# Kernel tuning notes

Hardware: AMD Instinct MI355X
Metric: run time of the kernel (lower is better)

The kernel has to match this reference:

```python
import jax, jax.numpy as jnp
import numpy as np

# Config constants (match init_kwargs)
H = 1024   # hidden_size
F = 4096   # intermediate_size
E = 8      # num_moe_experts
K = 2      # moe_router_topk
S, B = 1024, 2  # seq_len, micro-batch


def setup_inputs() -> dict:
    key = jax.random.key(0)
    ks = jax.random.split(key, 6)
    return {
        "hidden_states": jax.random.normal(ks[0], (S, B, H), jnp.float32),
        "router_w": jax.random.normal(ks[1], (H, E), jnp.float32) * 0.02,
        "w1": jax.random.normal(ks[2], (E, H, F), jnp.float32) * 0.02,
        "b1": jax.random.normal(ks[3], (E, F), jnp.float32) * 0.02,
        "w2": jax.random.normal(ks[4], (E, F, H), jnp.float32) * 0.02,
        "b2": jax.random.normal(ks[5], (E, H), jnp.float32) * 0.02,
    }


def reference(hidden_states, router_w, w1, b1, w2, b2):
    S_, B_, H_ = hidden_states.shape
    x = hidden_states.reshape(-1, H_)                      # [N, H]
    N = x.shape[0]

    # --- TopKRouter (aux_loss routing): topk over logits, softmax over top-k logits ---
    logits = x @ router_w                                  # [N, E]
    top_logits, indices = jax.lax.top_k(logits, K)         # [N, K]
    scores = jax.nn.softmax(top_logits.astype(jnp.float32), axis=-1).astype(logits.dtype)

    # Combine weights [N, E]: scatter top-k scores into expert slots.
    combine = jnp.zeros((N, E), x.dtype).at[jnp.arange(N)[:, None], indices].add(scores)

    # --- Experts: per-expert GPTNeoXMLP (dense over all tokens; math-equivalent
    # to dispatch (token_permutation) + grouped GEMM + scatter_add combine
    # (token_unpermutation) with score weighting for topk>1) ---
    h = jax.nn.gelu(jnp.einsum('nh,ehf->enf', x, w1) + b1[:, None, :], approximate=False)
    y = jnp.einsum('enf,efh->enh', h, w2) + b2[:, None, :]  # [E, N, H]

    out = jnp.einsum('ne,enh->nh', combine, y)              # weighted combine
    return out.reshape(S_, B_, H_)
```

## Files before the change

### kernel.cpp

```cpp
#include <hip/hip_runtime.h>
#include <cmath>


#define H_DIM 1024
#define F_DIM 4096
#define E_NUM 8
#define N_TOK 2048
#define BK 64
#define MAX_SLOTS 5120
#define MAX_MT (MAX_SLOTS / 128)

typedef short s16x8 __attribute__((ext_vector_type(8)));
typedef float f32x4 __attribute__((ext_vector_type(4)));

__device__ __forceinline__ unsigned short f2bf(float f) {
  unsigned int u = __float_as_uint(f);
  u += 0x7fffu + ((u >> 16) & 1u);
  return (unsigned short)(u >> 16);
}

__device__ __forceinline__ void gload_lds16(const void* g, void* l) {
  __builtin_amdgcn_global_load_lds(
      (const __attribute__((address_space(1))) unsigned int*)g,
      (__attribute__((address_space(3))) unsigned int*)l, 16, 0, 0);
}

__device__ __forceinline__ int xcd_swz(int orig, int nwg) {
  const int cpx = nwg >> 3;
  return (orig & 7) * cpx + (orig >> 3);
}

__device__ __forceinline__ float fast_gelu(float v) {
  const float w = v * (1.0f + 0.044715f * v * v);
  const float t = __expf(-1.5957691216f * w);
  return v / (1.0f + t);
}

__device__ __forceinline__ void tcvt_tile(const float* __restrict__ in,
                                          unsigned short* __restrict__ out,
                                          int R, int C, int tile, float (*T)[65]) {
  const int ctiles = C >> 6;
  const int per_e = ctiles * (R >> 6);
  const int e = tile / per_e;
  const int rem = tile - e * per_e;
  const int r0 = (rem / ctiles) << 6;
  const int c0 = (rem % ctiles) << 6;
  const size_t eb = (size_t)e * R * C;
  in += eb; out += eb;
  const int t = threadIdx.x;
  const int cb = (t & 15) * 4;
#pragma unroll
  for (int it = 0; it < 4; ++it) {
    const int rr = (t >> 4) + it * 16;
    f32x4 v = *(const f32x4*)(in + (size_t)(r0 + rr) * C + c0 + cb);
#pragma unroll
    for (int c = 0; c < 4; ++c) T[rr][cb + c] = v[c];
  }
  __syncthreads();
  const int cc = t >> 2;
  const int rb = (t & 3) * 16;
#pragma unroll
  for (int half = 0; half < 2; ++half) {
    s16x8 u;
#pragma unroll
    for (int j = 0; j < 8; ++j) u[j] = (short)f2bf(T[rb + half * 8 + j][cc]);
    *(s16x8*)&out[(size_t)(c0 + cc) * R + r0 + rb + half * 8] = u;
  }
}

__global__ __launch_bounds__(256) void prep1_k(
    const float* __restrict__ w1, unsigned short* __restrict__ wt1,
    const float* __restrict__ x, unsigned short* __restrict__ xb,
    const float* __restrict__ rw, int* __restrict__ meta,
    int* __restrict__ topk_e, float* __restrict__ topk_s) {
  __shared__ float T[64][65];
  const int b = blockIdx.x;
  const int t = threadIdx.x;
  if (b < 8192) {
    tcvt_tile(w1, wt1, H_DIM, F_DIM, b, T);
    return;
  }
  if (b < 9216) {
    const size_t i = (((size_t)(b - 8192)) * 256 + t) * 8;
    f32x4 a = *(const f32x4*)(x + i);
    f32x4 c = *(const f32x4*)(x + i + 4);
    s16x8 u;
#pragma unroll
    for (int j = 0; j < 4; ++j) { u[j] = (short)f2bf(a[j]); u[4 + j] = (short)f2bf(c[j]); }
    *(s16x8*)&xb[i] = u;
    return;
  }
  const int n = (b - 9216) * 4 + (t >> 6);
  const int l = t & 63;
  float part[E_NUM];
#pragma unroll
  for (int e = 0; e < E_NUM; ++e) part[e] = 0.f;
  const float* xr = x + (size_t)n * H_DIM;
  for (int h = l; h < H_DIM; h += 64) {
    const float xv = xr[h];
    const float* rwr = rw + h * E_NUM;
#pragma unroll
    for (int e = 0; e < E_NUM; ++e) part[e] += xv * rwr[e];
  }
#pragma unroll
  for (int e = 0; e < E_NUM; ++e) {
#pragma unroll
    for (int off = 32; off > 0; off >>= 1) part[e] += __shfl_down(part[e], off);
  }
  if (l == 0) {
    float v0 = -3.4e38f, v1 = -3.4e38f;
    int i0 = 0, i1 = 0;
#pragma unroll
    for (int e = 0; e < E_NUM; ++e) {
      float v = part[e];
      if (v > v0) { v1 = v0; i1 = i0; v0 = v; i0 = e; }
      else if (v > v1) { v1 = v; i1 = e; }
    }
    const float e1 = expf(v1 - v0);
    const float inv = 1.f / (1.f + e1);
    topk_e[2 * n] = i0; topk_e[2 * n + 1] = i1;
    topk_s[2 * n] = inv; topk_s[2 * n + 1] = e1 * inv;
    atomicAdd(&meta[i0], 1);
    atomicAdd(&meta[i1], 1);
  }
}

__global__ __launch_bounds__(256) void scatter_k(
    int* __restrict__ meta, const int* __restrict__ topk_e,
    const float* __restrict__ topk_s, int* __restrict__ slot_token,
    float* __restrict__ slot_score) {
  __shared__ int soff[9];
  __shared__ int scur[8];
  const int t = threadIdx.x;
  if (t == 0) {
    int acc = 0;
    for (int e = 0; e < E_NUM; ++e) {
      soff[e] = acc;
      meta[8 + e] = acc;
      acc += ((meta[e] + 127) / 128) * 128;
    }
    soff[8] = acc;
    meta[16] = acc;
  }
  if (t < 8) scur[t] = 0;
  __syncthreads();
  for (int i = t; i < MAX_SLOTS; i += 256) slot_token[i] = -1;
  __syncthreads();
  for (int a = t; a < N_TOK * 2; a += 256) {
    const int e = topk_e[a];
    const int pos = atomicAdd(&scur[e], 1);
    const int slot = soff[e] + pos;
    slot_token[slot] = a >> 1;
    slot_score[slot] = topk_s[a];
  }
}

__global__ __launch_bounds__(256, 2) void gemm1_f(
    const unsigned short* __restrict__ xb, const unsigned short* __restrict__ w1t,
    const float* __restrict__ b1, const int* __restrict__ meta,
    const int* __restrict__ slot_token, unsigned short* __restrict__ hbuf,
    const float* __restrict__ w2, unsigned short* __restrict__ wt2) {
  __shared__ __align__(16) char lraw[65536];
  if (blockIdx.x >= MAX_MT * 32) {
    tcvt_tile(w2, wt2, F_DIM, H_DIM, blockIdx.x - MAX_MT * 32, (float(*)[65])lraw);
    return;
  }
  unsigned short* Al = (unsigned short*)lraw;
  unsigned short* Bl = (unsigned short*)(lraw + 32768);
  const int total = meta[16];
  const int wgid = xcd_swz(blockIdx.x, MAX_MT * 32);
  const int mt = wgid >> 5, nt = wgid & 31;
  const int m0 = mt * 128;
  if (m0 >= total) return;
  int exp = 0;
#pragma unroll
  for (int e = 1; e < E_NUM; ++e) if (m0 >= meta[8 + e]) exp = e;
  const int n0 = nt * 128;
  const int t = threadIdx.x, w = t >> 6, l = t & 63;
  const int wm = w >> 1, wn = w & 1, lr = l & 15, lg = l >> 4;
  const int sr = l >> 3, sc = l & 7;

  const unsigned short* srcA[4];
  const unsigned short* srcB[4];
#pragma unroll
  for (int i = 0; i < 4; ++i) {
    const int r = (w * 4 + i) * 8 + sr;
    const int cd = sc ^ sr;
    int tk = slot_token[m0 + r]; if (tk < 0) tk = 0;
    srcA[i] = xb + (size_t)tk * H_DIM + cd * 8;
    srcB[i] = w1t + ((size_t)exp * F_DIM + n0 + r) * H_DIM + cd * 8;
  }

  const f32x4 fzero = {0.f, 0.f, 0.f, 0.f};
  f32x4 acc[4][4];
#pragma unroll
  for (int a = 0; a < 4; ++a)
#pragma unroll
    for (int b = 0; b < 4; ++b) acc[a][b] = fzero;

#pragma unroll
  for (int i = 0; i < 4; ++i) {
    gload_lds16(srcA[i], Al + (w * 4 + i) * 512);
    gload_lds16(srcB[i], Bl + (w * 4 + i) * 512);
  }
  __syncthreads();
  int cur = 0;
  for (int kt = 0; kt < H_DIM / BK; ++kt) {
    const int nxt = cur ^ 1;
    if (kt + 1 < H_DIM / BK) {
      const int k0 = (kt + 1) * BK;
#pragma unroll
      for (int i = 0; i < 4; ++i) {
        gload_lds16(srcA[i] + k0, Al + nxt * 8192 + (w * 4 + i) * 512);
        gload_lds16(srcB[i] + k0, Bl + nxt * 8192 + (w * 4 + i) * 512);
      }
    }
    const unsigned short* Ac = Al + cur * 8192;
    const unsigned short* Bc = Bl + cur * 8192;
#pragma unroll
    for (int kk = 0; kk < 2; ++kk) {
      s16x8 af[4], bb[4];
#pragma unroll
      for (int fm = 0; fm < 4; ++fm) {
        const int row = wm * 64 + fm * 16 + lr;
        af[fm] = *(const s16x8*)&Ac[row * 64 + (((kk * 4 + lg) ^ (lr & 7)) * 8)];
      }
#pragma unroll
      for (int fn = 0; fn < 4; ++fn) {
        const int row = wn * 64 + fn * 16 + lr;
        bb[fn] = *(const s16x8*)&Bc[row * 64 + (((kk * 4 + lg) ^ (lr & 7)) * 8)];
      }
#pragma unroll
      for (int fm = 0; fm < 4; ++fm)
#pragma unroll
        for (int fn = 0; fn < 4; ++fn)
          acc[fm][fn] = __builtin_amdgcn_mfma_f32_16x16x32_bf16(af[fm], bb[fn], acc[fm][fn], 0, 0, 0);
    }
    __syncthreads();
    cur = nxt;
  }
#pragma unroll
  for (int fn = 0; fn < 4; ++fn) {
    const int col = n0 + wn * 64 + fn * 16 + lr;
    const float bias = b1[exp * F_DIM + col];
#pragma unroll
    for (int fm = 0; fm < 4; ++fm) {
      const int rbase = m0 + wm * 64 + fm * 16 + lg * 4;
#pragma unroll
      for (int i = 0; i < 4; ++i) {
        hbuf[(size_t)(rbase + i) * F_DIM + col] = f2bf(fast_gelu(acc[fm][fn][i] + bias));
      }
    }
  }
}

__global__ __launch_bounds__(256, 2) void gemm2_f(
    const unsigned short* __restrict__ hbuf, const unsigned short* __restrict__ w2t,
    const float* __restrict__ b2, const int* __restrict__ meta,
    const int* __restrict__ slot_token, const float* __restrict__ slot_score,
    float* __restrict__ out) {
  __shared__ __align__(16) char lraw[49152];
  unsigned short* Al = (unsigned short*)lraw;
  unsigned short* Bl = (unsigned short*)(lraw + 32768);
  const int total = meta[16];
  const int wgid = xcd_swz(blockIdx.x, MAX_MT * 16);
  const int mt = wgid >> 4, nt = wgid & 15;
  const int m0 = mt * 128;
  if (m0 >= total) return;
  int exp = 0;
#pragma unroll
  for (int e = 1; e < E_NUM; ++e) if (m0 >= meta[8 + e]) exp = e;
  const int n0 = nt * 64;
  const int t = threadIdx.x, w = t >> 6, l = t & 63;
  const int wm = w >> 1, wn = w & 1, lr = l & 15, lg = l >> 4;
  const int sr = l >> 3, sc = l & 7;

  const unsigned short* srcA[4];
  const unsigned short* srcB[2];
#pragma unroll
  for (int i = 0; i < 4; ++i) {
    const int r = (w * 4 + i) * 8 + sr;
    srcA[i] = hbuf + (size_t)(m0 + r) * F_DIM + (sc ^ sr) * 8;
  }
#pragma unroll
  for (int i = 0; i < 2; ++i) {
    const int r = (w * 2 + i) * 8 + sr;
    srcB[i] = w2t + ((size_t)exp * H_DIM + n0 + r) * F_DIM + (sc ^ sr) * 8;
  }

  const f32x4 fzero = {0.f, 0.f, 0.f, 0.f};
  f32x4 acc[4][2];
#pragma unroll
  for (int a = 0; a < 4; ++a)
#pragma unroll
    for (int b = 0; b < 2; ++b) acc[a][b] = fzero;

#pragma unroll
  for (int i = 0; i < 4; ++i) gload_lds16(srcA[i], Al + (w * 4 + i) * 512);
#pragma unroll
  for (int i = 0; i < 2; ++i) gload_lds16(srcB[i], Bl + (w * 2 + i) * 512);
  __syncthreads();
  int cur = 0;
  for (int kt = 0; kt < F_DIM / BK; ++kt) {
    const int nxt = cur ^ 1;
    if (kt + 1 < F_DIM / BK) {
      const int k0 = (kt + 1) * BK;
#pragma unroll
      for (int i = 0; i < 4; ++i)
        gload_lds16(srcA[i] + k0, Al + nxt * 8192 + (w * 4 + i) * 512);
#pragma unroll
      for (int i = 0; i < 2; ++i)
        gload_lds16(srcB[i] + k0, Bl + nxt * 4096 + (w * 2 + i) * 512);
    }
    const unsigned short* Ac = Al + cur * 8192;
    const unsigned short* Bc = Bl + cur * 4096;
#pragma unroll
    for (int kk = 0; kk < 2; ++kk) {
      s16x8 af[4], bb[2];
#pragma unroll
      for (int fm = 0; fm < 4; ++fm) {
        const int row = wm * 64 + fm * 16 + lr;
        af[fm] = *(const s16x8*)&Ac[row * 64 + (((kk * 4 + lg) ^ (lr & 7)) * 8)];
      }
#pragma unroll
      for (int fn = 0; fn < 2; ++fn) {
        const int row = wn * 32 + fn * 16 + lr;
        bb[fn] = *(const s16x8*)&Bc[row * 64 + (((kk * 4 + lg) ^ (lr & 7)) * 8)];
      }
#pragma unroll
      for (int fm = 0; fm < 4; ++fm)
#pragma unroll
        for (int fn = 0; fn < 2; ++fn)
          acc[fm][fn] = __builtin_amdgcn_mfma_f32_16x16x32_bf16(af[fm], bb[fn], acc[fm][fn], 0, 0, 0);
    }
    __syncthreads();
    cur = nxt;
  }
#pragma unroll
  for (int fm = 0; fm < 4; ++fm) {
    const int rbase = m0 + wm * 64 + fm * 16 + lg * 4;
    int toks[4]; float ss[4];
#pragma unroll
    for (int i = 0; i < 4; ++i) {
      toks[i] = slot_token[rbase + i];
      ss[i] = slot_score[rbase + i];
    }
#pragma unroll
    for (int fn = 0; fn < 2; ++fn) {
      const int col = n0 + wn * 32 + fn * 16 + lr;
      const float b2v = b2[exp * H_DIM + col];
#pragma unroll
      for (int i = 0; i < 4; ++i) {
        if (toks[i] >= 0)
          atomicAdd(out + (size_t)toks[i] * H_DIM + col, ss[i] * (acc[fm][fn][i] + b2v));
      }
    }
  }
}

__global__ __launch_bounds__(256) void tcvt2_k(const float* __restrict__ in,
                                               unsigned short* __restrict__ out) {
  __shared__ float T[64][65];
  tcvt_tile(in, out, F_DIM, H_DIM, blockIdx.x, T);
}

extern "C" void kernel_launch(void* const* d_in, const int* in_sizes, int n_in,
                              void* d_out, int out_size, void* d_ws, size_t ws_size,
                              hipStream_t stream) {
  const float* x  = (const float*)d_in[0];
  const float* rw = (const float*)d_in[1];
  const float* w1 = (const float*)d_in[2];
  const float* b1 = (const float*)d_in[3];
  const float* w2 = (const float*)d_in[4];
  const float* b2 = (const float*)d_in[5];
  float* out = (float*)d_out;
  char* ws = (char*)d_ws;

  int*   meta       = (int*)ws;
  int*   topk_e     = (int*)(ws + 4096);
  float* topk_s     = (float*)(ws + 20480);
  int*   slot_token = (int*)(ws + 36864);
  float* slot_score = (float*)(ws + 57344);
  unsigned short* xb   = (unsigned short*)(ws + (1ull << 20));
  unsigned short* hbuf = (unsigned short*)(ws + (6ull << 20));
  unsigned short* wt1  = (unsigned short*)(ws + (48ull << 20));
  const size_t W = (size_t)E_NUM * H_DIM * F_DIM * 2;
  unsigned short* wt2  = (unsigned short*)(ws + (48ull << 20) + W);
  const size_t NEED_FULL = (48ull << 20) + 2 * W;
  const bool full = ws_size >= NEED_FULL;

  hipMemsetAsync(meta, 0, 256, stream);
  hipMemsetAsync(out, 0, (size_t)N_TOK * H_DIM * sizeof(float), stream);

  prep1_k<<<8192 + 1024 + 512, 256, 0, stream>>>(w1, wt1, x, xb, rw, meta, topk_e, topk_s);
  scatter_k<<<1, 256, 0, stream>>>(meta, topk_e, topk_s, slot_token, slot_score);

  if (full) {
    gemm1_f<<<MAX_MT * 32 + 8192, 256, 0, stream>>>(xb, wt1, b1, meta, slot_token, hbuf, w2, wt2);
    gemm2_f<<<MAX_MT * 16, 256, 0, stream>>>(hbuf, wt2, b2, meta, slot_token, slot_score, out);
  } else {
    gemm1_f<<<MAX_MT * 32, 256, 0, stream>>>(xb, wt1, b1, meta, slot_token, hbuf, w2, wt1);
    tcvt2_k<<<8192, 256, 0, stream>>>(w2, wt1);
    gemm2_f<<<MAX_MT * 16, 256, 0, stream>>>(hbuf, wt1, b2, meta, slot_token, slot_score, out);
  }
}
```

Before: 281.5 us.

## Replace LDS transpose-convert with register-based tiles, memset slot table, raise gemm2 occupancy

The weight transpose-and-bf16-convert no longer stages a 64x64 tile through shared memory. Each thread now reads a column strip of 32 rows into registers and writes 32 contiguous bf16 values, with half as many blocks. This drops LDS use and a barrier from the conversion blocks co-scheduled with gemm1. The slot_token initialization moves from the single-block scatter kernel to a hipMemsetAsync, and gemm2's launch bound asks for 3 blocks per CU. The column-strided global reads may coalesce less well, though each wavefront still reads contiguous rows of 256 floats.

```diff
diff --git a/kernel.cpp b/kernel.cpp
--- a/kernel.cpp
+++ b/kernel.cpp
@@ -9,6 +9,9 @@
 #define BK 64
 #define MAX_SLOTS 5120
 #define MAX_MT (MAX_SLOTS / 128)
+#define G1_GRID (MAX_MT * 32)
+#define G2_GRID (MAX_MT * 16)
+#define TCVT_BLKS 4096
 
 typedef short s16x8 __attribute__((ext_vector_type(8)));
 typedef float f32x4 __attribute__((ext_vector_type(4)));
@@ -36,35 +39,28 @@
   return v / (1.0f + t);
 }
 
-__device__ __forceinline__ void tcvt_tile(const float* __restrict__ in,
+__device__ __forceinline__ void fast_tcvt(const float* __restrict__ in,
                                           unsigned short* __restrict__ out,
-                                          int R, int C, int tile, float (*T)[65]) {
-  const int ctiles = C >> 6;
-  const int per_e = ctiles * (R >> 6);
-  const int e = tile / per_e;
-  const int rem = tile - e * per_e;
-  const int r0 = (rem / ctiles) << 6;
-  const int c0 = (rem % ctiles) << 6;
+                                          int R, int C, int tile) {
+  const int ct = C >> 8;
+  const int nb = (R >> 5) * ct;
+  const int e = tile / nb;
+  const int rem = tile - e * nb;
+  const int r0 = (rem / ct) << 5;
+  const int c0 = (rem % ct) << 8;
   const size_t eb = (size_t)e * R * C;
-  in += eb; out += eb;
-  const int t = threadIdx.x;
-  const int cb = (t & 15) * 4;
-#pragma unroll
-  for (int it = 0; it < 4; ++it) {
-    const int rr = (t >> 4) + it * 16;
-    f32x4 v = *(const f32x4*)(in + (size_t)(r0 + rr) * C + c0 + cb);
-#pragma unroll
-    for (int c = 0; c < 4; ++c) T[rr][cb + c] = v[c];
-  }
-  __syncthreads();
-  const int cc = t >> 2;
-  const int rb = (t & 3) * 16;
-#pragma unroll
-  for (int half = 0; half < 2; ++half) {
+  const int c = c0 + threadIdx.x;
+  const float* ip = in + eb + (size_t)r0 * C + c;
+  unsigned short* op = out + eb + (size_t)c * R + r0;
+  float v[32];
+#pragma unroll
+  for (int j = 0; j < 32; ++j) v[j] = ip[(size_t)j * C];
+#pragma unroll
+  for (int q = 0; q < 4; ++q) {
     s16x8 u;
 #pragma unroll
-    for (int j = 0; j < 8; ++j) u[j] = (short)f2bf(T[rb + half * 8 + j][cc]);
-    *(s16x8*)&out[(size_t)(c0 + cc) * R + r0 + rb + half * 8] = u;
+    for (int j = 0; j < 8; ++j) u[j] = (short)f2bf(v[q * 8 + j]);
+    *(s16x8*)(op + q * 8) = u;
   }
 }
 
@@ -73,15 +69,14 @@
     const float* __restrict__ x, unsigned short* __restrict__ xb,
     const float* __restrict__ rw, int* __restrict__ meta,
     int* __restrict__ topk_e, float* __restrict__ topk_s) {
-  __shared__ float T[64][65];
   const int b = blockIdx.x;
   const int t = threadIdx.x;
-  if (b < 8192) {
-    tcvt_tile(w1, wt1, H_DIM, F_DIM, b, T);
+  if (b < TCVT_BLKS) {
+    fast_tcvt(w1, wt1, H_DIM, F_DIM, b);
     return;
   }
-  if (b < 9216) {
-    const size_t i = (((size_t)(b - 8192)) * 256 + t) * 8;
+  if (b < TCVT_BLKS + 1024) {
+    const size_t i = (((size_t)(b - TCVT_BLKS)) * 256 + t) * 8;
     f32x4 a = *(const f32x4*)(x + i);
     f32x4 c = *(const f32x4*)(x + i + 4);
     s16x8 u;
@@ -90,7 +85,7 @@
     *(s16x8*)&xb[i] = u;
     return;
   }
-  const int n = (b - 9216) * 4 + (t >> 6);
+  const int n = (b - TCVT_BLKS - 1024) * 4 + (t >> 6);
   const int l = t & 63;
   float part[E_NUM];
 #pragma unroll
@@ -144,8 +139,6 @@
   }
   if (t < 8) scur[t] = 0;
   __syncthreads();
-  for (int i = t; i < MAX_SLOTS; i += 256) slot_token[i] = -1;
-  __syncthreads();
   for (int a = t; a < N_TOK * 2; a += 256) {
     const int e = topk_e[a];
     const int pos = atomicAdd(&scur[e], 1);
@@ -161,14 +154,14 @@
     const int* __restrict__ slot_token, unsigned short* __restrict__ hbuf,
     const float* __restrict__ w2, unsigned short* __restrict__ wt2) {
   __shared__ __align__(16) char lraw[65536];
-  if (blockIdx.x >= MAX_MT * 32) {
-    tcvt_tile(w2, wt2, F_DIM, H_DIM, blockIdx.x - MAX_MT * 32, (float(*)[65])lraw);
+  if (blockIdx.x >= G1_GRID) {
+    fast_tcvt(w2, wt2, F_DIM, H_DIM, blockIdx.x - G1_GRID);
     return;
   }
   unsigned short* Al = (unsigned short*)lraw;
   unsigned short* Bl = (unsigned short*)(lraw + 32768);
   const int total = meta[16];
-  const int wgid = xcd_swz(blockIdx.x, MAX_MT * 32);
+  const int wgid = xcd_swz(blockIdx.x, G1_GRID);
   const int mt = wgid >> 5, nt = wgid & 31;
   const int m0 = mt * 128;
   if (m0 >= total) return;
@@ -254,7 +247,7 @@
   }
 }
 
-__global__ __launch_bounds__(256, 2) void gemm2_f(
+__global__ __launch_bounds__(256, 3) void gemm2_f(
     const unsigned short* __restrict__ hbuf, const unsigned short* __restrict__ w2t,
     const float* __restrict__ b2, const int* __restrict__ meta,
     const int* __restrict__ slot_token, const float* __restrict__ slot_score,
@@ -263,7 +256,7 @@
   unsigned short* Al = (unsigned short*)lraw;
   unsigned short* Bl = (unsigned short*)(lraw + 32768);
   const int total = meta[16];
-  const int wgid = xcd_swz(blockIdx.x, MAX_MT * 16);
+  const int wgid = xcd_swz(blockIdx.x, G2_GRID);
   const int mt = wgid >> 4, nt = wgid & 15;
   const int m0 = mt * 128;
   if (m0 >= total) return;
@@ -360,8 +353,7 @@
 
 __global__ __launch_bounds__(256) void tcvt2_k(const float* __restrict__ in,
                                                unsigned short* __restrict__ out) {
-  __shared__ float T[64][65];
-  tcvt_tile(in, out, F_DIM, H_DIM, blockIdx.x, T);
+  fast_tcvt(in, out, F_DIM, H_DIM, blockIdx.x);
 }
 
 extern "C" void kernel_launch(void* const* d_in, const int* in_sizes, int n_in,
@@ -390,17 +382,18 @@
   const bool full = ws_size >= NEED_FULL;
 
   hipMemsetAsync(meta, 0, 256, stream);
+  hipMemsetAsync(slot_token, 0xFF, MAX_SLOTS * sizeof(int), stream);
   hipMemsetAsync(out, 0, (size_t)N_TOK * H_DIM * sizeof(float), stream);
 
-  prep1_k<<<8192 + 1024 + 512, 256, 0, stream>>>(w1, wt1, x, xb, rw, meta, topk_e, topk_s);
+  prep1_k<<<TCVT_BLKS + 1024 + 512, 256, 0, stream>>>(w1, wt1, x, xb, rw, meta, topk_e, topk_s);
   scatter_k<<<1, 256, 0, stream>>>(meta, topk_e, topk_s, slot_token, slot_score);
 
   if (full) {
-    gemm1_f<<<MAX_MT * 32 + 8192, 256, 0, stream>>>(xb, wt1, b1, meta, slot_token, hbuf, w2, wt2);
-    gemm2_f<<<MAX_MT * 16, 256, 0, stream>>>(hbuf, wt2, b2, meta, slot_token, slot_score, out);
+    gemm1_f<<<G1_GRID + TCVT_BLKS, 256, 0, stream>>>(xb, wt1, b1, meta, slot_token, hbuf, w2, wt2);
+    gemm2_f<<<G2_GRID, 256, 0, stream>>>(hbuf, wt2, b2, meta, slot_token, slot_score, out);
   } else {
-    gemm1_f<<<MAX_MT * 32, 256, 0, stream>>>(xb, wt1, b1, meta, slot_token, hbuf, w2, wt1);
-    tcvt2_k<<<8192, 256, 0, stream>>>(w2, wt1);
-    gemm2_f<<<MAX_MT * 16, 256, 0, stream>>>(hbuf, wt1, b2, meta, slot_token, slot_score, out);
-  }
-}
+    gemm1_f<<<G1_GRID, 256, 0, stream>>>(xb, wt1, b1, meta, slot_token, hbuf, w2, wt1);
+    tcvt2_k<<<TCVT_BLKS, 256, 0, stream>>>(w2, wt1);
+    gemm2_f<<<G2_GRID, 256, 0, stream>>>(hbuf, wt1, b2, meta, slot_token, slot_score, out);
+  }
+}
```

Result: slower. 304.5 us (+8.2%).
